# Optimization experiments

Measured on AMD Instinct MI355X. Metric: run time of the kernel, lower is better.

Reference implementation:

```python
import jax, jax.numpy as jnp
import numpy as np

NUM_LEVELS = 4
SEARCH_RADIUS = 4
EPS = 1e-12  # torch F.normalize eps


def _avg_pool2d(x, s):
    # avg pool with kernel=stride=s over last two dims (exact, since H,W divisible by s)
    lead = x.shape[:-2]
    H, W = x.shape[-2], x.shape[-1]
    x = x.reshape(*lead, H // s, s, W // s, s)
    return x.mean(axis=(-3, -1))


def _l2_normalize(x, axis):
    n = jnp.sqrt(jnp.sum(x * x, axis=axis, keepdims=True))
    return x / jnp.maximum(n, EPS)


def _compute_correlation(query, values, radius):
    # query: [B,C,H,W], values: [B,N,C,H,W] -> [B,N,H,W,(2r+1)^2]
    q = _l2_normalize(query, axis=1)
    v = _l2_normalize(values, axis=2)
    corrs = []
    for dy in range(-radius, radius + 1):
        for dx in range(-radius, radius + 1):
            vs = v if (dy == 0 and dx == 0) else jnp.roll(v, (dy, dx), axis=(-2, -1))
            corrs.append(jnp.einsum('bchw,bnchw->bnhw', q, vs))
    return jnp.stack(corrs, axis=-1)


def setup_inputs() -> dict:
    key = jax.random.key(0)
    k1, k2, k3, k4 = jax.random.split(key, 4)
    B, N, C, H, W = 2, 4, 128, 160, 160
    Co = C // 2
    return {
        'query_feat': jax.random.normal(k1, (B, C, H, W), dtype=jnp.float32),
        'value_feats': jax.random.normal(k2, (B, N, C, H, W), dtype=jnp.float32),
        'proj_w': jax.random.normal(k3, (Co, C), dtype=jnp.float32) * (1.0 / np.sqrt(C)),
        'proj_b': jax.random.normal(k4, (Co,), dtype=jnp.float32) * 0.01,
    }


def reference(query_feat, value_feats, proj_w, proj_b):
    # 1x1 conv projection C -> C//2
    q = jnp.einsum('oc,bchw->bohw', proj_w, query_feat) + proj_b[None, :, None, None]
    v = jnp.einsum('oc,bnchw->bnohw', proj_w, value_feats) + proj_b[None, None, :, None, None]
    outs = []
    for level in range(NUM_LEVELS):
        scale = 2 ** level
        radius = max(1, SEARCH_RADIUS // scale)
        if scale > 1:
            q_l = _avg_pool2d(q, scale)
            v_l = _avg_pool2d(v, scale)
        else:
            q_l, v_l = q, v
        outs.append(_compute_correlation(q_l, v_l, radius))
    return tuple(outs)
```

## Files before the change

### kernel.cpp

```cpp
#include <hip/hip_runtime.h>


typedef _Float16 f16;
typedef _Float16 f16x4 __attribute__((ext_vector_type(4)));
typedef _Float16 f16x8 __attribute__((ext_vector_type(8)));
typedef float f32x4 __attribute__((ext_vector_type(4)));

#define EPSN 1e-12f

#define XS 136

__global__ __launch_bounds__(256, 3) void proj_mfma(
    const float* __restrict__ xq, const float* __restrict__ xv,
    const float* __restrict__ wt, const float* __restrict__ bias,
    float* __restrict__ outf, f16* __restrict__ outh, int P) {
  __shared__ f16 xs[128 * XS];
  __shared__ f16 ws[64 * XS];

  int bid = blockIdx.x;
  int img = bid / 200;
  int p0 = (bid - img * 200) * 128;
  const float* xsrc = (img < 2) ? (xq + (size_t)img * 128 * P)
                                : (xv + (size_t)(img - 2) * 128 * P);

  int tid = threadIdx.x;
  int lane = tid & 63;
  int wv = tid >> 6;
  int cl = lane & 15;
  int quad = lane >> 4;

  for (int it = tid; it < 64 * 16; it += 256) {
    int o = it >> 4, g = it & 15;
    float4 w0 = *(const float4*)(wt + o * 128 + g * 8);
    float4 w1 = *(const float4*)(wt + o * 128 + g * 8 + 4);
    f16x8 h;
    h[0] = (f16)w0.x; h[1] = (f16)w0.y; h[2] = (f16)w0.z; h[3] = (f16)w0.w;
    h[4] = (f16)w1.x; h[5] = (f16)w1.y; h[6] = (f16)w1.z; h[7] = (f16)w1.w;
    *(f16x8*)(ws + o * XS + g * 8) = h;
  }

  {
    int pxs = tid & 127;
    int c0 = (tid >> 7) * 64;
    const float* xp = xsrc + (size_t)c0 * P + p0 + pxs;
    float v[64];
#pragma unroll
    for (int k = 0; k < 64; ++k) v[k] = xp[(size_t)k * P];
#pragma unroll
    for (int i = 0; i < 8; ++i) {
      f16x8 h;
#pragma unroll
      for (int k = 0; k < 8; ++k) h[k] = (f16)v[8 * i + k];
      *(f16x8*)(xs + pxs * XS + c0 + 8 * i) = h;
    }
  }
  __syncthreads();

  f32x4 acc[2][4];
#pragma unroll
  for (int a = 0; a < 2; ++a)
#pragma unroll
    for (int m = 0; m < 4; ++m) acc[a][m] = (f32x4)0.f;

#pragma unroll
  for (int kc = 0; kc < 4; ++kc) {
    f16x8 bfr[2], afr[4];
#pragma unroll
    for (int pt = 0; pt < 2; ++pt) {
      int px = (2 * wv + pt) * 16 + cl;
      bfr[pt] = *(const f16x8*)(xs + px * XS + kc * 32 + quad * 8);
    }
#pragma unroll
    for (int mt = 0; mt < 4; ++mt) {
      int o = mt * 16 + cl;
      afr[mt] = *(const f16x8*)(ws + o * XS + kc * 32 + quad * 8);
    }
#pragma unroll
    for (int pt = 0; pt < 2; ++pt)
#pragma unroll
      for (int mt = 0; mt < 4; ++mt)
        acc[pt][mt] = __builtin_amdgcn_mfma_f32_16x16x32_f16(afr[mt], bfr[pt], acc[pt][mt], 0, 0, 0);
  }

  float4 bi[4];
#pragma unroll
  for (int mt = 0; mt < 4; ++mt) bi[mt] = *(const float4*)(bias + mt * 16 + quad * 4);

#pragma unroll
  for (int pt = 0; pt < 2; ++pt) {
    int px = p0 + (2 * wv + pt) * 16 + cl;
    float ss = 0.f;
#pragma unroll
    for (int mt = 0; mt < 4; ++mt) {
      acc[pt][mt][0] += bi[mt].x;
      acc[pt][mt][1] += bi[mt].y;
      acc[pt][mt][2] += bi[mt].z;
      acc[pt][mt][3] += bi[mt].w;
#pragma unroll
      for (int r = 0; r < 4; ++r) ss = fmaf(acc[pt][mt][r], acc[pt][mt][r], ss);
    }
    ss += __shfl_xor(ss, 16, 64);
    ss += __shfl_xor(ss, 32, 64);
    float s = 1.0f / fmaxf(sqrtf(ss), EPSN);
    size_t base = ((size_t)img * P + px) * 64;
#pragma unroll
    for (int mt = 0; mt < 4; ++mt) {
      *(float4*)(outf + base + mt * 16 + quad * 4) =
          make_float4(acc[pt][mt][0], acc[pt][mt][1], acc[pt][mt][2], acc[pt][mt][3]);
      f16x4 hn;
      hn[0] = (f16)(acc[pt][mt][0] * s);
      hn[1] = (f16)(acc[pt][mt][1] * s);
      hn[2] = (f16)(acc[pt][mt][2] * s);
      hn[3] = (f16)(acc[pt][mt][3] * s);
      *(f16x4*)(outh + base + mt * 16 + quad * 4) = hn;
    }
  }
}

__global__ __launch_bounds__(256) void pool_all(
    const float* __restrict__ q0, f16* __restrict__ qh1,
    f16* __restrict__ qh2, f16* __restrict__ qh3) {
  int gid = blockIdx.x * 256 + threadIdx.x;
  int c4 = gid & 15;
  int g = (gid >> 4) & 3;
  int idx = gid >> 6;
  int w3 = idx % 20;
  int t = idx / 20;
  int h3 = t % 20;
  int img = t / 20;
  int h2 = 2 * h3 + (g >> 1);
  int w2 = 2 * w3 + (g & 1);

  const float4* in4 = (const float4*)q0;
  size_t base = ((size_t)(img * 160 + 4 * h2) * 160 + 4 * w2) * 16 + c4;
  float4 a[16];
#pragma unroll
  for (int i = 0; i < 4; ++i)
#pragma unroll
    for (int j = 0; j < 4; ++j)
      a[i * 4 + j] = in4[base + (size_t)i * 160 * 16 + j * 16];

  float4 v1[4];
  float4 q2v = make_float4(0.f, 0.f, 0.f, 0.f);
#pragma unroll
  for (int i1 = 0; i1 < 2; ++i1)
#pragma unroll
    for (int j1 = 0; j1 < 2; ++j1) {
      float4 s00 = a[(2 * i1) * 4 + 2 * j1];
      float4 s01 = a[(2 * i1) * 4 + 2 * j1 + 1];
      float4 s10 = a[(2 * i1 + 1) * 4 + 2 * j1];
      float4 s11 = a[(2 * i1 + 1) * 4 + 2 * j1 + 1];
      float4 r;
      r.x = 0.25f * (s00.x + s01.x + s10.x + s11.x);
      r.y = 0.25f * (s00.y + s01.y + s10.y + s11.y);
      r.z = 0.25f * (s00.z + s01.z + s10.z + s11.z);
      r.w = 0.25f * (s00.w + s01.w + s10.w + s11.w);
      v1[i1 * 2 + j1] = r;
      q2v.x += r.x; q2v.y += r.y; q2v.z += r.z; q2v.w += r.w;
    }
  q2v.x *= 0.25f; q2v.y *= 0.25f; q2v.z *= 0.25f; q2v.w *= 0.25f;

#pragma unroll
  for (int i1 = 0; i1 < 2; ++i1)
#pragma unroll
    for (int j1 = 0; j1 < 2; ++j1) {
      float4 r = v1[i1 * 2 + j1];
      float ss = fmaf(r.x, r.x, fmaf(r.y, r.y, fmaf(r.z, r.z, r.w * r.w)));
      ss += __shfl_xor(ss, 1, 64);
      ss += __shfl_xor(ss, 2, 64);
      ss += __shfl_xor(ss, 4, 64);
      ss += __shfl_xor(ss, 8, 64);
      float s = 1.0f / fmaxf(sqrtf(ss), EPSN);
      int y1 = 2 * h2 + i1, x1 = 2 * w2 + j1;
      f16x4 h;
      h[0] = (f16)(r.x * s); h[1] = (f16)(r.y * s);
      h[2] = (f16)(r.z * s); h[3] = (f16)(r.w * s);
      *(f16x4*)(qh1 + ((size_t)(img * 80 + y1) * 80 + x1) * 64 + c4 * 4) = h;
    }

  {
    float ss = fmaf(q2v.x, q2v.x, fmaf(q2v.y, q2v.y, fmaf(q2v.z, q2v.z, q2v.w * q2v.w)));
    ss += __shfl_xor(ss, 1, 64);
    ss += __shfl_xor(ss, 2, 64);
    ss += __shfl_xor(ss, 4, 64);
    ss += __shfl_xor(ss, 8, 64);
    float s = 1.0f / fmaxf(sqrtf(ss), EPSN);
    f16x4 h;
    h[0] = (f16)(q2v.x * s); h[1] = (f16)(q2v.y * s);
    h[2] = (f16)(q2v.z * s); h[3] = (f16)(q2v.w * s);
    *(f16x4*)(qh2 + ((size_t)(img * 40 + h2) * 40 + w2) * 64 + c4 * 4) = h;
  }

  {
    float4 q3v;
    q3v.x = q2v.x + __shfl_xor(q2v.x, 16, 64);
    q3v.y = q2v.y + __shfl_xor(q2v.y, 16, 64);
    q3v.z = q2v.z + __shfl_xor(q2v.z, 16, 64);
    q3v.w = q2v.w + __shfl_xor(q2v.w, 16, 64);
    q3v.x += __shfl_xor(q3v.x, 32, 64);
    q3v.y += __shfl_xor(q3v.y, 32, 64);
    q3v.z += __shfl_xor(q3v.z, 32, 64);
    q3v.w += __shfl_xor(q3v.w, 32, 64);
    q3v.x *= 0.25f; q3v.y *= 0.25f; q3v.z *= 0.25f; q3v.w *= 0.25f;
    float ss = fmaf(q3v.x, q3v.x, fmaf(q3v.y, q3v.y, fmaf(q3v.z, q3v.z, q3v.w * q3v.w)));
    ss += __shfl_xor(ss, 1, 64);
    ss += __shfl_xor(ss, 2, 64);
    ss += __shfl_xor(ss, 4, 64);
    ss += __shfl_xor(ss, 8, 64);
    float s = 1.0f / fmaxf(sqrtf(ss), EPSN);
    if (g == 0) {
      f16x4 h;
      h[0] = (f16)(q3v.x * s); h[1] = (f16)(q3v.y * s);
      h[2] = (f16)(q3v.z * s); h[3] = (f16)(q3v.w * s);
      *(f16x4*)(qh3 + ((size_t)(img * 20 + h3) * 20 + w3) * 64 + c4 * 4) = h;
    }
  }
}

template <int R>
__global__ __launch_bounds__(256, 8) void corr_mfma(
    const f16* __restrict__ qh, const f16* __restrict__ vh,
    float* __restrict__ out, int H, int W, int T) {
  constexpr int D = 2 * R + 1, DD = D * D;
  int bn = blockIdx.x & 7;
  int wv = threadIdx.x >> 6;
  int widx = (blockIdx.x >> 3) * 4 + wv;
  int h = widx / T;
  int wt = widx - h * T;
  int lane = threadIdx.x & 63;
  int cl = lane & 15, quad = lane >> 4;
  int b = bn >> 2;
  int w0 = wt * 16;

  int ap = w0 + cl; if (ap >= W) ap = W - 1;
  const f16* qp = qh + ((size_t)(b * H + h) * W + ap) * 64 + quad * 8;
  f16x8 a0 = *(const f16x8*)qp;
  f16x8 a1 = *(const f16x8*)(qp + 32);

  int c0 = w0 - R + cl; if (c0 < 0) c0 += W; if (c0 >= W) c0 -= W;
  int c1 = w0 + R + cl; if (c1 >= W) c1 -= W;
  int b0off = c0 * 64 + quad * 8;
  int b1off = c1 * 64 + quad * 8;

  int rbase = quad * 4;
  int base_dxi = rbase - cl + ((quad < 2) ? 2 * R : 0);
  int wr0 = w0 + rbase;
  int off0 = ((bn * H + h) * W + wr0) * DD + base_dxi;

  for (int dyi = 0; dyi < D; ++dyi) {
    int h2 = h - dyi + R; if (h2 < 0) h2 += H; else if (h2 >= H) h2 -= H;
    const f16* vrow = vh + ((size_t)(bn * H + h2) * W) * 64;
    f16x8 b0a = *(const f16x8*)(vrow + b0off);
    f16x8 b0b = *(const f16x8*)(vrow + b0off + 32);
    f16x8 b1a = *(const f16x8*)(vrow + b1off);
    f16x8 b1b = *(const f16x8*)(vrow + b1off + 32);
    f32x4 A0 = __builtin_amdgcn_mfma_f32_16x16x32_f16(a0, b0a, (f32x4)0.f, 0, 0, 0);
    A0 = __builtin_amdgcn_mfma_f32_16x16x32_f16(a1, b0b, A0, 0, 0, 0);
    f32x4 A1 = __builtin_amdgcn_mfma_f32_16x16x32_f16(a0, b1a, (f32x4)0.f, 0, 0, 0);
    A1 = __builtin_amdgcn_mfma_f32_16x16x32_f16(a1, b1b, A1, 0, 0, 0);
#pragma unroll
    for (int rr = 0; rr < 4; ++rr) {
      int dxi = base_dxi + rr;
      float val = (quad < 2) ? A0[rr] : A1[rr];
      if ((unsigned)dxi <= (unsigned)(2 * R) && (wr0 + rr) < W)
        out[off0 + dyi * D + rr * (DD + 1)] = val;
    }
  }
}

extern "C" void kernel_launch(void* const* d_in, const int* in_sizes, int n_in,
                              void* d_out, int out_size, void* d_ws, size_t ws_size,
                              hipStream_t stream) {
  const float* query  = (const float*)d_in[0];
  const float* values = (const float*)d_in[1];
  const float* pw     = (const float*)d_in[2];
  const float* pb     = (const float*)d_in[3];
  float* out = (float*)d_out;
  float* ws  = (float*)d_ws;

  const int B = 2, N = 4;
  const int P0 = 160 * 160;

  float* q0 = ws;
  f16* q0h = (f16*)(ws + (size_t)10 * P0 * 64);
  f16* v0h = q0h + (size_t)2 * P0 * 64;
  f16* qh1 = q0h + (size_t)10 * P0 * 64;
  f16* vh1 = qh1 + (size_t)2 * (P0 / 4) * 64;
  f16* qh2 = vh1 + (size_t)8 * (P0 / 4) * 64;
  f16* vh2 = qh2 + (size_t)2 * (P0 / 16) * 64;
  f16* qh3 = vh2 + (size_t)8 * (P0 / 16) * 64;
  f16* vh3 = qh3 + (size_t)2 * (P0 / 64) * 64;

  proj_mfma<<<2000, 256, 0, stream>>>(query, values, pw, pb, q0, q0h, P0);

  pool_all<<<1000, 256, 0, stream>>>(q0, qh1, qh2, qh3);

  float* out0 = out;
  float* out1 = out0 + (size_t)B * N * P0 * 81;
  float* out2 = out1 + (size_t)B * N * (P0 / 4) * 25;
  float* out3 = out2 + (size_t)B * N * (P0 / 16) * 9;
  corr_mfma<4><<<8 * 160 * 10 / 4, 256, 0, stream>>>(q0h, v0h, out0, 160, 160, 10);
  corr_mfma<2><<<8 * 80 * 5 / 4, 256, 0, stream>>>(qh1, vh1, out1, 80, 80, 5);
  corr_mfma<1><<<8 * 40 * 3 / 4, 256, 0, stream>>>(qh2, vh2, out2, 40, 40, 3);
  corr_mfma<1><<<8 * 20 * 2 / 4, 256, 0, stream>>>(qh3, vh3, out3, 20, 20, 2);
}
```

Before: 317.0 us.

## Load projection operands directly into MFMA fragments and pre-convert weights once

Removes the LDS staging of input pixels and weights from the projection kernel. Each lane now loads its f32 input channels straight from global memory into MFMA B-fragments, and reads f16 weights from a buffer converted once by a new prep_weights kernel. This drops the shared-memory round trip and the block barrier, and cuts the per-block weight conversion. The cost is an extra kernel launch, strided global loads that are only coalesced across 16 lanes, and weights now read from L2/global instead of LDS; occupancy hint raised to 4.

```diff
diff --git a/kernel.cpp b/kernel.cpp
--- a/kernel.cpp
+++ b/kernel.cpp
@@ -8,15 +8,19 @@
 
 #define EPSN 1e-12f
 
-#define XS 136
-
-__global__ __launch_bounds__(256, 3) void proj_mfma(
+__global__ __launch_bounds__(256) void prep_weights(
+    const float* __restrict__ wt, f16* __restrict__ wh) {
+  int gid = blockIdx.x * 256 + threadIdx.x;
+  float4 w = *(const float4*)(wt + gid * 4);
+  f16x4 h;
+  h[0] = (f16)w.x; h[1] = (f16)w.y; h[2] = (f16)w.z; h[3] = (f16)w.w;
+  *(f16x4*)(wh + gid * 4) = h;
+}
+
+__global__ __launch_bounds__(256, 4) void proj_mfma(
     const float* __restrict__ xq, const float* __restrict__ xv,
-    const float* __restrict__ wt, const float* __restrict__ bias,
+    const f16* __restrict__ wh, const float* __restrict__ bias,
     float* __restrict__ outf, f16* __restrict__ outh, int P) {
-  __shared__ f16 xs[128 * XS];
-  __shared__ f16 ws[64 * XS];
-
   int bid = blockIdx.x;
   int img = bid / 200;
   int p0 = (bid - img * 200) * 128;
@@ -29,32 +33,7 @@
   int cl = lane & 15;
   int quad = lane >> 4;
 
-  for (int it = tid; it < 64 * 16; it += 256) {
-    int o = it >> 4, g = it & 15;
-    float4 w0 = *(const float4*)(wt + o * 128 + g * 8);
-    float4 w1 = *(const float4*)(wt + o * 128 + g * 8 + 4);
-    f16x8 h;
-    h[0] = (f16)w0.x; h[1] = (f16)w0.y; h[2] = (f16)w0.z; h[3] = (f16)w0.w;
-    h[4] = (f16)w1.x; h[5] = (f16)w1.y; h[6] = (f16)w1.z; h[7] = (f16)w1.w;
-    *(f16x8*)(ws + o * XS + g * 8) = h;
-  }
-
-  {
-    int pxs = tid & 127;
-    int c0 = (tid >> 7) * 64;
-    const float* xp = xsrc + (size_t)c0 * P + p0 + pxs;
-    float v[64];
-#pragma unroll
-    for (int k = 0; k < 64; ++k) v[k] = xp[(size_t)k * P];
-#pragma unroll
-    for (int i = 0; i < 8; ++i) {
-      f16x8 h;
-#pragma unroll
-      for (int k = 0; k < 8; ++k) h[k] = (f16)v[8 * i + k];
-      *(f16x8*)(xs + pxs * XS + c0 + 8 * i) = h;
-    }
-  }
-  __syncthreads();
+  const float* xp = xsrc + (size_t)(quad * 8) * P + p0 + (2 * wv) * 16 + cl;
 
   f32x4 acc[2][4];
 #pragma unroll
@@ -64,22 +43,25 @@
 
 #pragma unroll
   for (int kc = 0; kc < 4; ++kc) {
-    f16x8 bfr[2], afr[4];
-#pragma unroll
-    for (int pt = 0; pt < 2; ++pt) {
-      int px = (2 * wv + pt) * 16 + cl;
-      bfr[pt] = *(const f16x8*)(xs + px * XS + kc * 32 + quad * 8);
-    }
+    float v0[8], v1[8];
+#pragma unroll
+    for (int k = 0; k < 8; ++k) {
+      const float* c = xp + (size_t)(kc * 32 + k) * P;
+      v0[k] = c[0];
+      v1[k] = c[16];
+    }
+    f16x8 b0, b1;
+#pragma unroll
+    for (int k = 0; k < 8; ++k) { b0[k] = (f16)v0[k]; b1[k] = (f16)v1[k]; }
+    f16x8 afr[4];
+#pragma unroll
+    for (int mt = 0; mt < 4; ++mt)
+      afr[mt] = *(const f16x8*)(wh + (mt * 16 + cl) * 128 + kc * 32 + quad * 8);
 #pragma unroll
     for (int mt = 0; mt < 4; ++mt) {
-      int o = mt * 16 + cl;
-      afr[mt] = *(const f16x8*)(ws + o * XS + kc * 32 + quad * 8);
-    }
-#pragma unroll
-    for (int pt = 0; pt < 2; ++pt)
-#pragma unroll
-      for (int mt = 0; mt < 4; ++mt)
-        acc[pt][mt] = __builtin_amdgcn_mfma_f32_16x16x32_f16(afr[mt], bfr[pt], acc[pt][mt], 0, 0, 0);
+      acc[0][mt] = __builtin_amdgcn_mfma_f32_16x16x32_f16(afr[mt], b0, acc[0][mt], 0, 0, 0);
+      acc[1][mt] = __builtin_amdgcn_mfma_f32_16x16x32_f16(afr[mt], b1, acc[1][mt], 0, 0, 0);
+    }
   }
 
   float4 bi[4];
@@ -290,8 +272,11 @@
   f16* vh2 = qh2 + (size_t)2 * (P0 / 16) * 64;
   f16* qh3 = vh2 + (size_t)8 * (P0 / 16) * 64;
   f16* vh3 = qh3 + (size_t)2 * (P0 / 64) * 64;
-
-  proj_mfma<<<2000, 256, 0, stream>>>(query, values, pw, pb, q0, q0h, P0);
+  f16* wh  = vh3 + (size_t)8 * (P0 / 64) * 64;
+
+  prep_weights<<<8, 256, 0, stream>>>(pw, wh);
+
+  proj_mfma<<<2000, 256, 0, stream>>>(query, values, wh, pb, q0, q0h, P0);
 
   pool_all<<<1000, 256, 0, stream>>>(q0, qh1, qh2, qh3);
 
```

Result: slower. 332.9 us (+5.0%).
